# Optimization experiments

Hardware: AMD Instinct MI355X
Metric: run time of the kernel (lower is better)

The kernel has to match this reference:

```python
import jax, jax.numpy as jnp
import numpy as np

D_MODEL = 4096
RANK = 16
BATCH = 4
SEQ = 4096


def setup_inputs() -> dict:
    key = jax.random.key(0)
    k_x, k_w, k_b, k_a, k_bb = jax.random.split(key, 5)
    x = jax.random.normal(k_x, (BATCH, SEQ, D_MODEL), dtype=jnp.float32)
    W = jax.random.normal(k_w, (D_MODEL, D_MODEL), dtype=jnp.float32) * 0.02
    bias = jax.random.normal(k_b, (D_MODEL,), dtype=jnp.float32) * 0.02
    A = jax.random.normal(k_a, (D_MODEL, RANK), dtype=jnp.float32) * 0.01
    B = jax.random.normal(k_bb, (RANK, D_MODEL), dtype=jnp.float32) * 0.01
    return {"x": x, "W": W, "bias": bias, "A": A, "B": B}


def reference(x, W, bias, A, B):
    # Faithful to the torch module: delta_W = A @ B; linear(x, W + delta_W, bias)
    # i.e. out = x @ (W + A @ B)^T + bias, with W: [d_out, d_in], x: [b, s, d_in].
    delta_W = A @ B                                   # [d_out, d_in]
    out = jnp.einsum("bsi,oi->bso", x, W + delta_W) + bias
    return out
```

## Files before the change

### kernel.cpp

```cpp
#include <hip/hip_runtime.h>
#include <stdint.h>


#define MDIM 16384
#define NDIM 4096
#define KDIM 4096
#define RANK 16
#define NT   (KDIM / 64)

typedef __bf16  bf16x8 __attribute__((ext_vector_type(8)));
typedef float   f32x4  __attribute__((ext_vector_type(4)));
typedef unsigned short u16x8 __attribute__((ext_vector_type(8)));

__device__ __forceinline__ unsigned short f2bf(float f) {
  union { float f; uint32_t u; } v; v.f = f;
  uint32_t r = v.u + 0x7FFFu + ((v.u >> 16) & 1u);
  return (unsigned short)(r >> 16);
}

__device__ __forceinline__ void gl16(const void* g, void* l) {
  __builtin_amdgcn_global_load_lds(
      (__attribute__((address_space(1))) void*)(g),
      (__attribute__((address_space(3))) void*)(l),
      16, 0, 0);
}

#define CAST_BLOCKS 32768
__global__ void prep_fused(const float* __restrict__ x,
                           const float* __restrict__ W,
                           const float* __restrict__ A,
                           const float* __restrict__ Bm,
                           unsigned short* __restrict__ xb,
                           unsigned short* __restrict__ Wp) {
  const int b = blockIdx.x;
  if (b < CAST_BLOCKS) {
    const size_t i = ((size_t)b * 256 + threadIdx.x) * 8;
    float4 a0 = *(const float4*)(x + i);
    float4 a1 = *(const float4*)(x + i + 4);
    u16x8 o;
    o[0] = f2bf(a0.x); o[1] = f2bf(a0.y); o[2] = f2bf(a0.z); o[3] = f2bf(a0.w);
    o[4] = f2bf(a1.x); o[5] = f2bf(a1.y); o[6] = f2bf(a1.z); o[7] = f2bf(a1.w);
    *(u16x8*)(xb + i) = o;
  } else {
    const size_t idx = ((size_t)(b - CAST_BLOCKS) * 256 + threadIdx.x) * 8;
    const int o  = (int)(idx >> 12);
    const int i0 = (int)(idx & 4095);
    float accv[8];
    {
      float4 w0 = *(const float4*)(W + (size_t)o * NDIM + i0);
      float4 w1 = *(const float4*)(W + (size_t)o * NDIM + i0 + 4);
      accv[0] = w0.x; accv[1] = w0.y; accv[2] = w0.z; accv[3] = w0.w;
      accv[4] = w1.x; accv[5] = w1.y; accv[6] = w1.z; accv[7] = w1.w;
    }
#pragma unroll
    for (int r = 0; r < RANK; ++r) {
      const float ar = A[o * RANK + r];
      float4 b0 = *(const float4*)(Bm + (size_t)r * NDIM + i0);
      float4 b1 = *(const float4*)(Bm + (size_t)r * NDIM + i0 + 4);
      accv[0] += ar * b0.x; accv[1] += ar * b0.y;
      accv[2] += ar * b0.z; accv[3] += ar * b0.w;
      accv[4] += ar * b1.x; accv[5] += ar * b1.y;
      accv[6] += ar * b1.z; accv[7] += ar * b1.w;
    }
    u16x8 ov;
#pragma unroll
    for (int j = 0; j < 8; ++j) ov[j] = f2bf(accv[j]);
    *(u16x8*)(Wp + idx) = ov;
  }
}

#define BARRIER  __builtin_amdgcn_s_barrier()
#define VMCNT8   asm volatile("s_waitcnt vmcnt(8)" ::: "memory")
#define VMCNT6   asm volatile("s_waitcnt vmcnt(6)" ::: "memory")
#define WAITVM0  asm volatile("s_waitcnt vmcnt(0)" ::: "memory")
#define LGKM0    asm volatile("s_waitcnt lgkmcnt(0)" ::: "memory")
#define SCHEDB   __builtin_amdgcn_sched_barrier(0)

#define DSR(dst, addr, imm)                                                   \
  asm volatile("ds_read_b128 %0, %1 offset:%c2"                               \
               : "=v"(dst) : "v"(addr), "n"(imm) : "memory")

#define STAGE_A(buf, h, kt) do {                                              \
    const int kc_ = ((kt) < NT ? (kt) : NT - 1);                              \
    const unsigned short* g_ = agb + (size_t)((h) * 64) * KDIM + kc_ * 64;    \
    unsigned short* d_ = &sA[(buf)][0] + (h) * 8192 + t * 8;                  \
    gl16(g_, d_);                                                             \
    gl16(g_ + (size_t)128 * KDIM, d_ + 4096);                                 \
  } while (0)

#define STAGE_B(buf, h, kt) do {                                              \
    const int kc_ = ((kt) < NT ? (kt) : NT - 1);                              \
    const unsigned short* g_ = bgb + (size_t)((h) * 32) * KDIM + kc_ * 64;    \
    unsigned short* d_ = &sB[(buf)][0] + (h) * 8192 + t * 8;                  \
    gl16(g_, d_);                                                             \
    gl16(g_ + (size_t)128 * KDIM, d_ + 4096);                                 \
  } while (0)

#define LDA(buf, mh) do {                                                     \
    DSR(a[0][0], aAddr0, (buf)*32768 + (mh)*16384 + 0);                       \
    DSR(a[0][1], aAddr1, (buf)*32768 + (mh)*16384 + 0);                       \
    DSR(a[1][0], aAddr0, (buf)*32768 + (mh)*16384 + 2048);                    \
    DSR(a[1][1], aAddr1, (buf)*32768 + (mh)*16384 + 2048);                    \
    DSR(a[2][0], aAddr0, (buf)*32768 + (mh)*16384 + 4096);                    \
    DSR(a[2][1], aAddr1, (buf)*32768 + (mh)*16384 + 4096);                    \
    DSR(a[3][0], aAddr0, (buf)*32768 + (mh)*16384 + 6144);                    \
    DSR(a[3][1], aAddr1, (buf)*32768 + (mh)*16384 + 6144);                    \
  } while (0)

#define LDB(bb, buf, nh) do {                                                 \
    DSR(bb[0][0], bAddr0, (buf)*32768 + (nh)*16384 + 0);                      \
    DSR(bb[0][1], bAddr1, (buf)*32768 + (nh)*16384 + 0);                      \
    DSR(bb[1][0], bAddr0, (buf)*32768 + (nh)*16384 + 2048);                   \
    DSR(bb[1][1], bAddr1, (buf)*32768 + (nh)*16384 + 2048);                   \
  } while (0)

#define MM(mh, nh, bb) do {                                                   \
    __builtin_amdgcn_s_setprio(1);                                            \
    _Pragma("unroll") for (int mi = 0; mi < 4; ++mi)                          \
    _Pragma("unroll") for (int ni = 0; ni < 2; ++ni)                          \
    _Pragma("unroll") for (int kk = 0; kk < 2; ++kk)                          \
      acc[(mh)*4+mi][(nh)*2+ni] = __builtin_amdgcn_mfma_f32_16x16x32_bf16(    \
          a[mi][kk], bb[ni][kk], acc[(mh)*4+mi][(nh)*2+ni], 0, 0, 0);         \
    __builtin_amdgcn_s_setprio(0);                                            \
  } while (0)

__global__ __launch_bounds__(512, 2) void gemm256(
    const unsigned short* __restrict__ Xb,
    const unsigned short* __restrict__ Wp,
    const float* __restrict__ bias,
    float* __restrict__ out) {
  __shared__ __align__(16) unsigned short sA[2][256 * 64];
  __shared__ __align__(16) unsigned short sB[2][256 * 64];

  const int t  = threadIdx.x;
  const int l  = t & 63;
  const int w  = t >> 6;
  const int wm = w >> 2;
  const int wn = w & 3;

  const int bid = blockIdx.x;
  const int swz = (bid & 7) * (1024 / 8) + (bid >> 3);
  const int bm  = (swz >> 4) * 256;
  const int bn  = (swz & 15) * 256;

  const int sr  = t >> 3;
  const int ske = (((t & 7) * 16) ^ ((sr & 7) << 4)) >> 1;
  const unsigned short* agb = Xb + (size_t)(bm + sr) * KDIM + ske;
  const unsigned short* bgb = Wp + (size_t)(bn + (sr >> 5) * 64 + (sr & 31)) * KDIM + ske;

  const int lr   = l & 15;
  const int koff = (l >> 4) * 8;
  const int xorE = (lr & 7) << 3;
  const unsigned ldsA = (unsigned)(uintptr_t)&sA[0][0];
  const unsigned ldsB = (unsigned)(uintptr_t)&sB[0][0];
  const unsigned aAddr0 = ldsA + (unsigned)((wm * 64 + lr) * 128 + ((koff ^ xorE) * 2));
  const unsigned aAddr1 = ldsA + (unsigned)((wm * 64 + lr) * 128 + (((32 + koff) ^ xorE) * 2));
  const unsigned bAddr0 = ldsB + (unsigned)((wn * 32 + lr) * 128 + ((koff ^ xorE) * 2));
  const unsigned bAddr1 = ldsB + (unsigned)((wn * 32 + lr) * 128 + (((32 + koff) ^ xorE) * 2));

  bf16x8 a[4][2], b0[2][2], b1[2][2];
  f32x4 acc[8][4];
#pragma unroll
  for (int i = 0; i < 8; ++i)
#pragma unroll
    for (int j = 0; j < 4; ++j)
      acc[i][j] = f32x4{0.f, 0.f, 0.f, 0.f};

  STAGE_A(0, 0, 0); STAGE_B(0, 0, 0); STAGE_A(0, 1, 0); STAGE_B(0, 1, 0);
  STAGE_A(1, 0, 1); STAGE_B(1, 0, 1); STAGE_B(1, 1, 1);
  VMCNT6;
  BARRIER;

  for (int it = 0; it < NT / 2; ++it) {
    const int E = it * 2;
    LDA(0, 0); LDB(b0, 0, 0);
    STAGE_A(1, 1, E + 1);
    BARRIER; LGKM0; SCHEDB;
    MM(0, 0, b0);
    BARRIER;
    LDB(b1, 0, 1);
    STAGE_A(0, 0, E + 2);
    BARRIER; LGKM0; SCHEDB;
    MM(0, 1, b1);
    VMCNT8;
    BARRIER;
    LDA(0, 1);
    STAGE_B(0, 0, E + 2);
    BARRIER; LGKM0; SCHEDB;
    MM(1, 1, b1);
    BARRIER;
    STAGE_B(0, 1, E + 2);
    BARRIER;
    MM(1, 0, b0);
    VMCNT8;
    BARRIER;
    LDA(1, 0); LDB(b0, 1, 0);
    STAGE_A(0, 1, E + 2);
    BARRIER; LGKM0; SCHEDB;
    MM(0, 0, b0);
    BARRIER;
    LDB(b1, 1, 1);
    STAGE_A(1, 0, E + 3);
    BARRIER; LGKM0; SCHEDB;
    MM(0, 1, b1);
    VMCNT8;
    BARRIER;
    LDA(1, 1);
    STAGE_B(1, 0, E + 3);
    BARRIER; LGKM0; SCHEDB;
    MM(1, 1, b1);
    BARRIER;
    STAGE_B(1, 1, E + 3);
    BARRIER;
    MM(1, 0, b0);
    VMCNT8;
    BARRIER;
  }

  WAITVM0;

#pragma unroll
  for (int mf = 0; mf < 8; ++mf) {
#pragma unroll
    for (int nf = 0; nf < 4; ++nf) {
      const int row = bm + wm * 128 + mf * 16 + (l >> 4) * 4;
      const int col = bn + wn * 64 + nf * 16 + lr;
      const float bv = bias[col];
#pragma unroll
      for (int r = 0; r < 4; ++r)
        out[(size_t)(row + r) * NDIM + col] = acc[mf][nf][r] + bv;
    }
  }
}

extern "C" void kernel_launch(void* const* d_in, const int* in_sizes, int n_in,
                              void* d_out, int out_size, void* d_ws, size_t ws_size,
                              hipStream_t stream) {
  const float* x    = (const float*)d_in[0];
  const float* W    = (const float*)d_in[1];
  const float* bias = (const float*)d_in[2];
  const float* A    = (const float*)d_in[3];
  const float* B    = (const float*)d_in[4];
  float* out        = (float*)d_out;

  unsigned short* Wp = (unsigned short*)d_ws;
  unsigned short* Xb = (unsigned short*)d_ws + (size_t)NDIM * KDIM;

  prep_fused<<<dim3(CAST_BLOCKS + 8192), 256, 0, stream>>>(x, W, A, B, Xb, Wp);
  gemm256<<<dim3((MDIM / 256) * (NDIM / 256)), 512, 0, stream>>>(Xb, Wp, bias, out);
}
```

Measured before the change: 596.2 us.

## Overlap LDS reads with MFMAs via staged lgkmcnt waits and early B-fragment prefetch

Replaces the full lgkmcnt(0) wait before each MFMA block with graduated lgkmcnt waits, so each A-row or B-column slice of MFMAs starts as soon as its LDS reads land. The B fragment for the next phase is prefetched at the end of the previous phase instead of at the start, and extra vmcnt waits are inserted to keep the global-to-LDS pipeline correct. This is meant to hide LDS read latency behind matrix work. The cost is more fragile ordering that depends on the asm-level counter assumptions, and the extra vmcnt waits could stall more often.

```diff
diff --git a/kernel.cpp b/kernel.cpp
--- a/kernel.cpp
+++ b/kernel.cpp
@@ -73,8 +73,11 @@
 #define VMCNT8   asm volatile("s_waitcnt vmcnt(8)" ::: "memory")
 #define VMCNT6   asm volatile("s_waitcnt vmcnt(6)" ::: "memory")
 #define WAITVM0  asm volatile("s_waitcnt vmcnt(0)" ::: "memory")
-#define LGKM0    asm volatile("s_waitcnt lgkmcnt(0)" ::: "memory")
+#define LGKMC_(n) asm volatile("s_waitcnt lgkmcnt(" #n ")" ::: "memory")
+#define LGKMC(n) LGKMC_(n)
 #define SCHEDB   __builtin_amdgcn_sched_barrier(0)
+#define PRIO1    __builtin_amdgcn_s_setprio(1)
+#define PRIO0    __builtin_amdgcn_s_setprio(0)
 
 #define DSR(dst, addr, imm)                                                   \
   asm volatile("ds_read_b128 %0, %1 offset:%c2"                               \
@@ -114,15 +117,37 @@
     DSR(bb[1][1], bAddr1, (buf)*32768 + (nh)*16384 + 2048);                   \
   } while (0)
 
-#define MM(mh, nh, bb) do {                                                   \
-    __builtin_amdgcn_s_setprio(1);                                            \
+#define MMmi(mh, nh, mi, bb) do {                                             \
+    _Pragma("unroll") for (int ni = 0; ni < 2; ++ni)                          \
+    _Pragma("unroll") for (int kk = 0; kk < 2; ++kk)                          \
+      acc[(mh)*4+(mi)][(nh)*2+ni] = __builtin_amdgcn_mfma_f32_16x16x32_bf16(  \
+          a[mi][kk], bb[ni][kk], acc[(mh)*4+(mi)][(nh)*2+ni], 0, 0, 0);       \
+  } while (0)
+
+#define MMni(mh, nh, ni, bb) do {                                             \
+    _Pragma("unroll") for (int mi = 0; mi < 4; ++mi)                          \
+    _Pragma("unroll") for (int kk = 0; kk < 2; ++kk)                          \
+      acc[(mh)*4+mi][(nh)*2+(ni)] = __builtin_amdgcn_mfma_f32_16x16x32_bf16(  \
+          a[mi][kk], bb[ni][kk], acc[(mh)*4+mi][(nh)*2+(ni)], 0, 0, 0);       \
+  } while (0)
+
+#define MMfull(mh, nh, bb) do {                                               \
     _Pragma("unroll") for (int mi = 0; mi < 4; ++mi)                          \
     _Pragma("unroll") for (int ni = 0; ni < 2; ++ni)                          \
     _Pragma("unroll") for (int kk = 0; kk < 2; ++kk)                          \
       acc[(mh)*4+mi][(nh)*2+ni] = __builtin_amdgcn_mfma_f32_16x16x32_bf16(    \
           a[mi][kk], bb[ni][kk], acc[(mh)*4+mi][(nh)*2+ni], 0, 0, 0);         \
-    __builtin_amdgcn_s_setprio(0);                                            \
-  } while (0)
+  } while (0)
+
+#define PH_A(bb, mh, nh)                                                      \
+    PRIO1; LGKMC(6); SCHEDB; MMmi(mh, nh, 0, bb);                             \
+    LGKMC(4); SCHEDB; MMmi(mh, nh, 1, bb);                                    \
+    LGKMC(2); SCHEDB; MMmi(mh, nh, 2, bb);                                    \
+    LGKMC(0); SCHEDB; MMmi(mh, nh, 3, bb); PRIO0
+
+#define PH_B(bb, mh, nh)                                                      \
+    PRIO1; LGKMC(2); SCHEDB; MMni(mh, nh, 0, bb);                             \
+    LGKMC(0); SCHEDB; MMni(mh, nh, 1, bb); PRIO0
 
 __global__ __launch_bounds__(512, 2) void gemm256(
     const unsigned short* __restrict__ Xb,
@@ -170,53 +195,61 @@
   STAGE_A(1, 0, 1); STAGE_B(1, 0, 1); STAGE_B(1, 1, 1);
   VMCNT6;
   BARRIER;
+  LDB(b0, 0, 0);
 
   for (int it = 0; it < NT / 2; ++it) {
     const int E = it * 2;
-    LDA(0, 0); LDB(b0, 0, 0);
+    LDA(0, 0);
     STAGE_A(1, 1, E + 1);
-    BARRIER; LGKM0; SCHEDB;
-    MM(0, 0, b0);
+    BARRIER;
+    PH_A(b0, 0, 0);
+    VMCNT8;
     BARRIER;
     LDB(b1, 0, 1);
     STAGE_A(0, 0, E + 2);
-    BARRIER; LGKM0; SCHEDB;
-    MM(0, 1, b1);
+    BARRIER;
+    PH_B(b1, 0, 1);
     VMCNT8;
     BARRIER;
     LDA(0, 1);
     STAGE_B(0, 0, E + 2);
-    BARRIER; LGKM0; SCHEDB;
-    MM(1, 1, b1);
+    BARRIER;
+    PH_A(b1, 1, 1);
+    VMCNT8;
     BARRIER;
     STAGE_B(0, 1, E + 2);
     BARRIER;
-    MM(1, 0, b0);
-    VMCNT8;
-    BARRIER;
-    LDA(1, 0); LDB(b0, 1, 0);
+    PRIO1; MMfull(1, 0, b0); PRIO0;
+    LDB(b0, 1, 0);
+    VMCNT8;
+    BARRIER;
+    LDA(1, 0);
     STAGE_A(0, 1, E + 2);
-    BARRIER; LGKM0; SCHEDB;
-    MM(0, 0, b0);
+    BARRIER;
+    PH_A(b0, 0, 0);
+    VMCNT8;
     BARRIER;
     LDB(b1, 1, 1);
     STAGE_A(1, 0, E + 3);
-    BARRIER; LGKM0; SCHEDB;
-    MM(0, 1, b1);
+    BARRIER;
+    PH_B(b1, 0, 1);
     VMCNT8;
     BARRIER;
     LDA(1, 1);
     STAGE_B(1, 0, E + 3);
-    BARRIER; LGKM0; SCHEDB;
-    MM(1, 1, b1);
+    BARRIER;
+    PH_A(b1, 1, 1);
+    VMCNT8;
     BARRIER;
     STAGE_B(1, 1, E + 3);
     BARRIER;
-    MM(1, 0, b0);
+    PRIO1; MMfull(1, 0, b0); PRIO0;
+    LDB(b0, 0, 0);
     VMCNT8;
     BARRIER;
   }
 
+  LGKMC(0);
   WAITVM0;
 
 #pragma unroll
```

Result: no change. 601.2 us (+0.8%).
